# Kernel tuning notes

Measured on AMD Instinct MI355X. Metric: run time of the kernel, lower is better.

## Reference

```python
import jax, jax.numpy as jnp
import numpy as np

D_MODEL = 1024
N_HEADS = 16
HEAD_DIM = D_MODEL // N_HEADS
LN_EPS = 1e-6


def setup_inputs() -> dict:
    key = jax.random.key(0)
    ks = jax.random.split(key, 10)
    B, L, D = 4, 1024, D_MODEL
    s = 1.0 / np.sqrt(D)
    return {
        "q": jax.random.normal(ks[0], (B, L, D), jnp.float32),
        "k": jax.random.normal(ks[1], (B, L, D), jnp.float32),
        "v": jax.random.normal(ks[2], (B, L, D), jnp.float32),
        "masks": jnp.zeros((B, L, L), jnp.bool_),
        "Wq": jax.random.normal(ks[3], (D, D), jnp.float32) * s,
        "bq": jnp.zeros((D,), jnp.float32),
        "Wk": jax.random.normal(ks[4], (D, D), jnp.float32) * s,
        "bk": jnp.zeros((D,), jnp.float32),
        "Wv": jax.random.normal(ks[5], (D, D), jnp.float32) * s,
        "bv": jnp.zeros((D,), jnp.float32),
        "ln_g": jnp.ones((D,), jnp.float32),
        "ln_b": jnp.zeros((D,), jnp.float32),
    }


def _layer_norm(x, g, b):
    mu = jnp.mean(x, axis=-1, keepdims=True)
    var = jnp.var(x, axis=-1, keepdims=True)
    return (x - mu) * jax.lax.rsqrt(var + LN_EPS) * g + b


def reference(q, k, v, masks, Wq, bq, Wk, bk, Wv, bv, ln_g, ln_b):
    B, Lq, D = q.shape
    Lk = k.shape[1]
    H, Dh = N_HEADS, HEAD_DIM
    # linear projections (nn.Linear: x @ W.T + b)
    qp = q @ Wq.T + bq  # [B, Lq, D]
    kp = k @ Wk.T + bk
    vp = v @ Wv.T + bv
    # split heads: [B, L, D] -> [B, H, L, Dh]
    qh = qp.reshape(B, Lq, H, Dh).transpose(0, 2, 1, 3)
    kh = kp.reshape(B, Lk, H, Dh).transpose(0, 2, 1, 3)
    vh = vp.reshape(B, Lk, H, Dh).transpose(0, 2, 1, 3)
    scores = jnp.einsum("bhqd,bhkd->bhqk", qh, kh) / jnp.sqrt(jnp.float32(Dh))
    scores = jnp.where(masks[:, None, :, :], -jnp.inf, scores)
    attention = jax.nn.softmax(scores, axis=-1)  # [B, H, Lq, Lk]
    ctx = jnp.einsum("bhqk,bhkd->bhqd", attention, vh)  # [B, H, Lq, Dh]
    ctx = ctx.transpose(0, 2, 1, 3).reshape(B, Lq, D)  # unmulti_head
    output = _layer_norm(qp + ctx, ln_g, ln_b)  # residual is projected q
    return output, attention.reshape(B * H, Lq, Lk)
```

## Files before the change

### kernel.cpp

```cpp
#include <hip/hip_runtime.h>
#include <hip/hip_bf16.h>

typedef short bf16x8 __attribute__((ext_vector_type(8)));
typedef short bf16x4 __attribute__((ext_vector_type(4)));
typedef float f32x4 __attribute__((ext_vector_type(4)));
typedef unsigned short u16x8 __attribute__((ext_vector_type(8)));
typedef unsigned short u16x4 __attribute__((ext_vector_type(4)));

#define DEV static __device__ __forceinline__

DEV unsigned short f2bf(float f) {
  unsigned int u = __builtin_bit_cast(unsigned int, f);
  u += 0x7FFFu + ((u >> 16) & 1u);
  return (unsigned short)(u >> 16);
}
DEV float bf2f(unsigned short u) {
  return __builtin_bit_cast(float, (unsigned int)u << 16);
}

DEV void gload_lds16(const unsigned short* g, unsigned short* l) {
  __builtin_amdgcn_global_load_lds(
      (const __attribute__((address_space(1))) unsigned int*)g,
      (__attribute__((address_space(3))) unsigned int*)l, 16, 0, 0);
}

DEV void waitv(int n) {
  switch (n) {
    case 0: asm volatile("s_waitcnt vmcnt(0)" ::: "memory"); break;
    case 1: asm volatile("s_waitcnt vmcnt(1)" ::: "memory"); break;
    case 2: asm volatile("s_waitcnt vmcnt(2)" ::: "memory"); break;
    case 3: asm volatile("s_waitcnt vmcnt(3)" ::: "memory"); break;
    case 4: asm volatile("s_waitcnt vmcnt(4)" ::: "memory"); break;
    case 5: asm volatile("s_waitcnt vmcnt(5)" ::: "memory"); break;
    case 6: asm volatile("s_waitcnt vmcnt(6)" ::: "memory"); break;
    default: asm volatile("s_waitcnt vmcnt(0)" ::: "memory"); break;
  }
}

#define SB() __builtin_amdgcn_sched_barrier(0)
#define BAR() do { __builtin_amdgcn_s_barrier(); SB(); } while (0)
#define LBAR() do { asm volatile("s_waitcnt lgkmcnt(0)" ::: "memory"); \
                    SB(); \
                    __builtin_amdgcn_s_barrier(); \
                    SB(); } while (0)
#define WAITL() do { asm volatile("s_waitcnt lgkmcnt(0)" ::: "memory"); SB(); } while (0)
#define PRIO1() __builtin_amdgcn_s_setprio(1)
#define PRIO0() __builtin_amdgcn_s_setprio(0)

DEV void amask(unsigned mwv, f32x4& s) {
  if (mwv) {
#pragma unroll
    for (int r = 0; r < 4; ++r)
      if ((mwv >> (8 * r)) & 0xffu) s[r] = -1.0e30f;
  }
}

__global__ __launch_bounds__(256) void cvt_kernel(
    const float* __restrict__ q, const float* __restrict__ k,
    const float* __restrict__ v, const float* __restrict__ wq,
    const float* __restrict__ wk, const float* __restrict__ wv,
    unsigned short* __restrict__ xq, unsigned short* __restrict__ xk,
    unsigned short* __restrict__ xv, unsigned short* __restrict__ wqb,
    unsigned short* __restrict__ wkb, unsigned short* __restrict__ wvb)
{
  int tid = blockIdx.x * 256 + threadIdx.x;
  const float* src; unsigned short* dst; int off;
  if      (tid <  524288) { src = q;  dst = xq;  off = tid; }
  else if (tid < 1048576) { src = k;  dst = xk;  off = tid -  524288; }
  else if (tid < 1572864) { src = v;  dst = xv;  off = tid - 1048576; }
  else if (tid < 1703936) { src = wq; dst = wqb; off = tid - 1572864; }
  else if (tid < 1835008) { src = wk; dst = wkb; off = tid - 1703936; }
  else                    { src = wv; dst = wvb; off = tid - 1835008; }
  size_t e = (size_t)off * 8;
  float4 a = *(const float4*)(src + e);
  float4 b = *(const float4*)(src + e + 4);
  u16x8 p = { f2bf(a.x), f2bf(a.y), f2bf(a.z), f2bf(a.w),
              f2bf(b.x), f2bf(b.y), f2bf(b.z), f2bf(b.w) };
  *(u16x8*)(dst + e) = p;
}

__global__ __launch_bounds__(512, 2) void gemm_kernel(
    const unsigned short* __restrict__ xq, const unsigned short* __restrict__ xk,
    const unsigned short* __restrict__ xv, const unsigned short* __restrict__ wqb,
    const unsigned short* __restrict__ wkb, const unsigned short* __restrict__ wvb,
    const float* __restrict__ bq, const float* __restrict__ bk,
    const float* __restrict__ bv, unsigned short* __restrict__ qp,
    unsigned short* __restrict__ kp, unsigned short* __restrict__ vt)
{
  __shared__ union {
    unsigned short ab[2][2][128][64];
    unsigned short T[128][132];
  } smu;
  const int t = threadIdx.x, lane = t & 63, wv8 = t >> 6;
  const int ln = lane & 15, g = lane >> 4;
  const int wm2 = wv8 >> 2, wn4 = wv8 & 3;
  const int seg = blockIdx.x >> 8, lb = blockIdx.x & 255;
  const int x8 = lb & 7, s32 = lb >> 3;
  const int m0 = (x8 * 4 + (s32 >> 3)) * 128;
  const int n0 = (s32 & 7) * 128;

  const unsigned short* X; const unsigned short* W; const float* bias;
  unsigned short* outR; int mode;
  if (seg == 0)      { X = xq; W = wqb; bias = bq; outR = qp; mode = 0; }
  else if (seg == 1) { X = xk; W = wkb; bias = bk; outR = kp; mode = 0; }
  else               { X = xv; W = wvb; bias = bv; outR = vt; mode = 2; }

  f32x4 acc[4][2];
#pragma unroll
  for (int i = 0; i < 4; ++i)
#pragma unroll
    for (int j = 0; j < 2; ++j) acc[i][j] = {0.f, 0.f, 0.f, 0.f};

  const int lrow = lane >> 3;
  const int lcol = ((lane & 7) ^ lrow) * 8;

#define STAGE_G(kt) do { \
    const int _k0 = (kt) * 64; \
    _Pragma("unroll") \
    for (int i = 0; i < 2; ++i) { \
      const int r = wv8 * 16 + i * 8; \
      gload_lds16(X + (size_t)(m0 + r + lrow) * 1024 + _k0 + lcol, \
                  &smu.ab[(kt) & 1][0][r][0]); \
      gload_lds16(W + (size_t)(n0 + r + lrow) * 1024 + _k0 + lcol, \
                  &smu.ab[(kt) & 1][1][r][0]); \
    } } while (0)

  STAGE_G(0);
  waitv(0);
  BAR();
#pragma unroll 2
  for (int kt = 0; kt < 16; ++kt) {
    if (kt < 15) STAGE_G(kt + 1);
    SB();
#pragma unroll
    for (int ks = 0; ks < 2; ++ks) {
      bf16x8 af[4], bfr[2];
      const int ru = ((ks * 4 + g) ^ (ln & 7)) * 8;
#pragma unroll
      for (int i = 0; i < 4; ++i)
        af[i] = *(const bf16x8*)&smu.ab[kt & 1][0][wm2 * 64 + i * 16 + ln][ru];
#pragma unroll
      for (int j = 0; j < 2; ++j)
        bfr[j] = *(const bf16x8*)&smu.ab[kt & 1][1][wn4 * 32 + j * 16 + ln][ru];
      PRIO1();
#pragma unroll
      for (int i = 0; i < 4; ++i)
#pragma unroll
        for (int j = 0; j < 2; ++j)
          acc[i][j] = __builtin_amdgcn_mfma_f32_16x16x32_bf16(
              af[i], bfr[j], acc[i][j], 0, 0, 0);
      PRIO0();
    }
    SB();
    waitv(0);
    BAR();
  }

  float bvv[2];
#pragma unroll
  for (int j = 0; j < 2; ++j) bvv[j] = bias[n0 + wn4 * 32 + j * 16 + ln];

  if (mode == 0) {
#pragma unroll
    for (int i = 0; i < 4; ++i)
#pragma unroll
      for (int j = 0; j < 2; ++j)
#pragma unroll
        for (int r = 0; r < 4; ++r) {
          int row = m0 + wm2 * 64 + i * 16 + g * 4 + r;
          int col = n0 + wn4 * 32 + j * 16 + ln;
          outR[(size_t)row * 1024 + col] = f2bf(acc[i][j][r] + bvv[j]);
        }
  } else {
    __syncthreads();
#pragma unroll
    for (int i = 0; i < 4; ++i)
#pragma unroll
      for (int j = 0; j < 2; ++j)
#pragma unroll
        for (int r = 0; r < 4; ++r)
          smu.T[wn4 * 32 + j * 16 + ln][wm2 * 64 + i * 16 + g * 4 + r] =
              f2bf(acc[i][j][r] + bvv[j]);
    __syncthreads();
    const int bb = m0 >> 10, l0 = m0 & 1023;
#pragma unroll
    for (int it = 0; it < 4; ++it) {
      const int col = it * 32 + (t >> 4);
      const int r8 = (t & 15) * 8;
      *(u16x8*)&outR[((size_t)(bb * 16 + (n0 >> 6) + (col >> 6)) * 64 + (col & 63)) * 1024 + l0 + r8] =
          *(const u16x8*)&smu.T[col][r8];
    }
  }
#undef STAGE_G
}

__global__ __launch_bounds__(512, 2) void attn_kernel(
    const unsigned short* __restrict__ qp, const unsigned short* __restrict__ kp,
    const unsigned short* __restrict__ vt, const unsigned char* __restrict__ masks,
    float* __restrict__ attn_out, float* __restrict__ res_out)
{
  __shared__ union {
    unsigned short Kw[8][3][1024];
    unsigned short Vb[3][64][128];
    float ctxp[4][32][68];
  } sm;
  __shared__ float red[2][2][16][4];

  const int t = threadIdx.x;
  const int wv = t >> 6, lane = t & 63;
  const int ln = lane & 15, g = lane >> 4;
  const int wq = wv & 3, wm = wv >> 2;
  const int hw = blockIdx.x;
  const int lid = (hw & 7) * 256 + (hw >> 3);
  const int b = lid >> 9, h = (lid >> 5) & 15, m0 = (lid & 31) * 32;
  const size_t rowbase = (size_t)(b * 1024 + m0);

  bf16x8 qf[2];
  {
    const unsigned short* qb =
        qp + (rowbase + wm * 16 + ln) * 1024 + h * 64 + g * 8;
    qf[0] = *(const bf16x8*)qb;
    qf[1] = *(const bf16x8*)(qb + 32);
  }
  SB();

  const int slr8 = lane >> 3;
  const int suK = (lane & 7) ^ slr8;
  const int vlr = lane >> 4;
  const int vu1 = (lane & 15) ^ vlr;
  const int vu2 = (lane & 15) ^ (4 + vlr);
  const unsigned short* kbase = kp + (size_t)b * 1048576 + h * 64;
  const unsigned short* vtb = vt + ((size_t)(b * 16 + h) * 64) * 1024;
  unsigned short* kwv = &sm.Kw[wv][0][0];

#define STAGE_K(tt) do { \
    gload_lds16(kbase + (size_t)((tt) * 64 + wq * 16 + slr8) * 1024 + suK * 8, \
                kwv + ((tt) % 3) * 1024); \
    gload_lds16(kbase + (size_t)((tt) * 64 + wq * 16 + 8 + slr8) * 1024 + suK * 8, \
                kwv + ((tt) % 3) * 1024 + 512); } while (0)
#define STAGE_V(c) do { \
    gload_lds16(vtb + (size_t)(wv * 8 + vlr) * 1024 + (c) * 128 + vu1 * 8, \
                &sm.Vb[(c) % 3][wv * 8][0]); \
    gload_lds16(vtb + (size_t)(wv * 8 + 4 + vlr) * 1024 + (c) * 128 + vu2 * 8, \
                &sm.Vb[(c) % 3][wv * 8 + 4][0]); } while (0)

  f32x4 sc[16];
#pragma unroll
  for (int i = 0; i < 16; ++i) sc[i] = {0.f, 0.f, 0.f, 0.f};

  STAGE_K(0); STAGE_K(1); STAGE_K(2);
  SB();
#pragma unroll
  for (int tt = 0; tt < 16; ++tt) {
    waitv(tt <= 13 ? 4 : (tt == 14 ? 2 : 0));
    SB();
    const unsigned short* ksl = kwv + (tt % 3) * 1024 + ln * 64;
    bf16x8 kf0 = *(const bf16x8*)(ksl + (g ^ (ln & 7)) * 8);
    bf16x8 kf1 = *(const bf16x8*)(ksl + ((4 + g) ^ (ln & 7)) * 8);
    WAITL();
    if (tt + 3 < 16) STAGE_K(tt + 3);
    SB();
    PRIO1();
    sc[tt] = __builtin_amdgcn_mfma_f32_16x16x32_bf16(kf0, qf[0], sc[tt], 0, 0, 0);
    sc[tt] = __builtin_amdgcn_mfma_f32_16x16x32_bf16(kf1, qf[1], sc[tt], 0, 0, 0);
    PRIO0();
  }

  unsigned mw[16];
  {
    const unsigned char* mrow =
        masks + ((size_t)b * 1024 + m0 + wm * 16 + ln) * 1024 + wq * 16 + g * 4;
#pragma unroll
    for (int tt = 0; tt < 16; ++tt) mw[tt] = *(const unsigned*)(mrow + tt * 64);
  }
  SB();

  LBAR();
  STAGE_V(0); STAGE_V(1);
  SB();

  const float C = 0.18033688011112042f;
  float mx = -3.0e30f;
#pragma unroll
  for (int tt = 0; tt < 16; ++tt) {
    amask(mw[tt], sc[tt]);
#pragma unroll
    for (int r = 0; r < 4; ++r) mx = fmaxf(mx, sc[tt][r]);
  }
  mx = fmaxf(mx, __shfl_xor(mx, 16));
  mx = fmaxf(mx, __shfl_xor(mx, 32));
  const float mtl = mx * C;
  float sum = 0.f;
#pragma unroll
  for (int tt = 0; tt < 16; ++tt)
#pragma unroll
    for (int r = 0; r < 4; ++r)
      sum += exp2f(__builtin_fmaf(sc[tt][r], C, -mtl));
  sum += __shfl_xor(sum, 16);
  sum += __shfl_xor(sum, 32);
  if (g == 0) { red[0][wm][ln][wq] = mx; red[1][wm][ln][wq] = sum; }
  LBAR();
  float m4 = fmaxf(fmaxf(red[0][wm][ln][0], red[0][wm][ln][1]),
                   fmaxf(red[0][wm][ln][2], red[0][wm][ln][3]));
  float l4 = 0.f;
#pragma unroll
  for (int i = 0; i < 4; ++i)
    l4 += red[1][wm][ln][i] * exp2f((red[0][wm][ln][i] - m4) * C);
  const float beta = __builtin_fmaf(-m4, C, -__builtin_log2f(l4));

  bf16x8 af8[8];
#pragma unroll
  for (int c = 0; c < 8; ++c) {
    bf16x8 a;
#pragma unroll
    for (int r = 0; r < 4; ++r)
      a[r] = (short)f2bf(exp2f(__builtin_fmaf(sc[2 * c][r], C, beta)));
#pragma unroll
    for (int r = 0; r < 4; ++r)
      a[4 + r] = (short)f2bf(exp2f(__builtin_fmaf(sc[2 * c + 1][r], C, beta)));
    af8[c] = a;
  }

  f32x4 cacc[4];
#pragma unroll
  for (int i = 0; i < 4; ++i) cacc[i] = {0.f, 0.f, 0.f, 0.f};
#pragma unroll
  for (int c = 0; c < 8; ++c) {
    waitv(c <= 6 ? 2 : 0);
    BAR();
    if (c + 2 < 8) STAGE_V(c + 2);
    SB();
#pragma unroll
    for (int ni = 0; ni < 4; ++ni) {
      const int d = ni * 16 + ln;
      const int u0 = (2 * wq + (g >> 1)) ^ (ln & 7);
      const int u1 = (8 + 2 * wq + (g >> 1)) ^ (ln & 7);
      bf16x4 b0 = *(const bf16x4*)&sm.Vb[c % 3][d][u0 * 8 + (g & 1) * 4];
      bf16x4 b1 = *(const bf16x4*)&sm.Vb[c % 3][d][u1 * 8 + (g & 1) * 4];
      bf16x8 bfr = { b0[0], b0[1], b0[2], b0[3], b1[0], b1[1], b1[2], b1[3] };
      PRIO1();
      cacc[ni] = __builtin_amdgcn_mfma_f32_16x16x32_bf16(af8[c], bfr, cacc[ni], 0, 0, 0);
      PRIO0();
    }
    SB();
  }

  LBAR();
#pragma unroll
  for (int ni = 0; ni < 4; ++ni)
#pragma unroll
    for (int r = 0; r < 4; ++r)
      sm.ctxp[wq][wm * 16 + g * 4 + r][ni * 16 + ln] = cacc[ni][r];
  LBAR();
  {
    const int m = t >> 4, d4 = (t & 15) * 4;
    f32x4 s0 = *(const f32x4*)&sm.ctxp[0][m][d4];
    f32x4 s1 = *(const f32x4*)&sm.ctxp[1][m][d4];
    f32x4 s2 = *(const f32x4*)&sm.ctxp[2][m][d4];
    f32x4 s3 = *(const f32x4*)&sm.ctxp[3][m][d4];
    f32x4 s = s0 + s1 + s2 + s3;
    const unsigned short* qrow = qp + (rowbase + m) * 1024 + h * 64 + d4;
    u16x4 qv = *(const u16x4*)qrow;
    f32x4 qf32 = { bf2f(qv[0]), bf2f(qv[1]), bf2f(qv[2]), bf2f(qv[3]) };
    s = s + qf32;
    *(f32x4*)(res_out + (rowbase + m) * 1024 + h * 64 + d4) = s;
  }
  SB();

  {
    const size_t abase =
        ((size_t)(b * 16 + h) * 1024 + (m0 + wm * 16 + ln)) * 1024 + wq * 16 + g * 4;
#pragma unroll
    for (int c = 0; c < 8; ++c)
#pragma unroll
      for (int hf = 0; hf < 2; ++hf) {
        f32x4 v = { bf2f((unsigned short)af8[c][hf * 4 + 0]),
                    bf2f((unsigned short)af8[c][hf * 4 + 1]),
                    bf2f((unsigned short)af8[c][hf * 4 + 2]),
                    bf2f((unsigned short)af8[c][hf * 4 + 3]) };
        *(f32x4*)(attn_out + abase + (2 * c + hf) * 64) = v;
      }
  }
#undef STAGE_K
#undef STAGE_V
}

__global__ __launch_bounds__(256) void ln_kernel(
    float* __restrict__ io,
    const float* __restrict__ gma, const float* __restrict__ bta)
{
  __shared__ float rbuf[2][4];
  const int r = blockIdx.x, t = threadIdx.x;
  const int i4 = t * 4;
  const size_t base = (size_t)r * 1024 + i4;
  f32x4 x = *(const f32x4*)(io + base);
  float s = x[0] + x[1] + x[2] + x[3];
  float q = x[0]*x[0] + x[1]*x[1] + x[2]*x[2] + x[3]*x[3];
#pragma unroll
  for (int off = 1; off < 64; off <<= 1) {
    s += __shfl_xor(s, off);
    q += __shfl_xor(q, off);
  }
  const int wv = t >> 6;
  if ((t & 63) == 0) { rbuf[0][wv] = s; rbuf[1][wv] = q; }
  __syncthreads();
  s = rbuf[0][0] + rbuf[0][1] + rbuf[0][2] + rbuf[0][3];
  q = rbuf[1][0] + rbuf[1][1] + rbuf[1][2] + rbuf[1][3];
  float mu = s * (1.0f / 1024.0f);
  float var = q * (1.0f / 1024.0f) - mu * mu;
  float is = rsqrtf(var + 1e-6f);
  f32x4 gv = *(const f32x4*)(gma + i4);
  f32x4 bv = *(const f32x4*)(bta + i4);
  f32x4 o;
#pragma unroll
  for (int k = 0; k < 4; ++k) o[k] = (x[k] - mu) * is * gv[k] + bv[k];
  *(f32x4*)(io + base) = o;
}

extern "C" void kernel_launch(void* const* d_in, const int* in_sizes, int n_in,
                              void* d_out, int out_size, void* d_ws, size_t ws_size,
                              hipStream_t stream) {
  const float* q  = (const float*)d_in[0];
  const float* k  = (const float*)d_in[1];
  const float* v  = (const float*)d_in[2];
  const unsigned char* masks = (const unsigned char*)d_in[3];
  const float* Wq = (const float*)d_in[4];
  const float* bq = (const float*)d_in[5];
  const float* Wk = (const float*)d_in[6];
  const float* bk = (const float*)d_in[7];
  const float* Wv = (const float*)d_in[8];
  const float* bv = (const float*)d_in[9];
  const float* lg = (const float*)d_in[10];
  const float* lb = (const float*)d_in[11];

  float* out = (float*)d_out;
  float* attn_out = out + (size_t)4 * 1024 * 1024;

  unsigned short* xq  = (unsigned short*)attn_out;
  unsigned short* xk  = xq + 4194304;
  unsigned short* xv  = xk + 4194304;
  unsigned short* wqb = xv + 4194304;
  unsigned short* wkb = wqb + 1048576;
  unsigned short* wvb = wkb + 1048576;

  unsigned short* qp = (unsigned short*)d_ws;
  unsigned short* kp = qp + 4194304;
  unsigned short* vt = kp + 4194304;

  hipLaunchKernelGGL(cvt_kernel, dim3(7680), dim3(256), 0, stream,
                     q, k, v, Wq, Wk, Wv, xq, xk, xv, wqb, wkb, wvb);
  hipLaunchKernelGGL(gemm_kernel, dim3(768), dim3(512), 0, stream,
                     xq, xk, xv, wqb, wkb, wvb, bq, bk, bv, qp, kp, vt);
  hipLaunchKernelGGL(attn_kernel, dim3(2048), dim3(512), 0, stream,
                     qp, kp, vt, masks, attn_out, out);
  hipLaunchKernelGGL(ln_kernel, dim3(4096), dim3(256), 0, stream,
                     out, lg, lb);
}
```

Measured before the change: 184.4 us.

## Fuse activation bf16 conversion into GEMM loads and interleave attention-prob stores

```diff
diff --git a/kernel.cpp b/kernel.cpp
--- a/kernel.cpp
+++ b/kernel.cpp
@@ -55,22 +55,16 @@
   }
 }
 
-__global__ __launch_bounds__(256) void cvt_kernel(
-    const float* __restrict__ q, const float* __restrict__ k,
-    const float* __restrict__ v, const float* __restrict__ wq,
-    const float* __restrict__ wk, const float* __restrict__ wv,
-    unsigned short* __restrict__ xq, unsigned short* __restrict__ xk,
-    unsigned short* __restrict__ xv, unsigned short* __restrict__ wqb,
+__global__ __launch_bounds__(256) void cvtw_kernel(
+    const float* __restrict__ wq, const float* __restrict__ wk,
+    const float* __restrict__ wv, unsigned short* __restrict__ wqb,
     unsigned short* __restrict__ wkb, unsigned short* __restrict__ wvb)
 {
   int tid = blockIdx.x * 256 + threadIdx.x;
   const float* src; unsigned short* dst; int off;
-  if      (tid <  524288) { src = q;  dst = xq;  off = tid; }
-  else if (tid < 1048576) { src = k;  dst = xk;  off = tid -  524288; }
-  else if (tid < 1572864) { src = v;  dst = xv;  off = tid - 1048576; }
-  else if (tid < 1703936) { src = wq; dst = wqb; off = tid - 1572864; }
-  else if (tid < 1835008) { src = wk; dst = wkb; off = tid - 1703936; }
-  else                    { src = wv; dst = wvb; off = tid - 1835008; }
+  if      (tid < 131072) { src = wq; dst = wqb; off = tid; }
+  else if (tid < 262144) { src = wk; dst = wkb; off = tid - 131072; }
+  else                   { src = wv; dst = wvb; off = tid - 262144; }
   size_t e = (size_t)off * 8;
   float4 a = *(const float4*)(src + e);
   float4 b = *(const float4*)(src + e + 4);
@@ -80,8 +74,8 @@
 }
 
 __global__ __launch_bounds__(512, 2) void gemm_kernel(
-    const unsigned short* __restrict__ xq, const unsigned short* __restrict__ xk,
-    const unsigned short* __restrict__ xv, const unsigned short* __restrict__ wqb,
+    const float* __restrict__ xq, const float* __restrict__ xk,
+    const float* __restrict__ xv, const unsigned short* __restrict__ wqb,
     const unsigned short* __restrict__ wkb, const unsigned short* __restrict__ wvb,
     const float* __restrict__ bq, const float* __restrict__ bk,
     const float* __restrict__ bv, unsigned short* __restrict__ qp,
@@ -99,7 +93,7 @@
   const int m0 = (x8 * 4 + (s32 >> 3)) * 128;
   const int n0 = (s32 & 7) * 128;
 
-  const unsigned short* X; const unsigned short* W; const float* bias;
+  const float* X; const unsigned short* W; const float* bias;
   unsigned short* outR; int mode;
   if (seg == 0)      { X = xq; W = wqb; bias = bq; outR = qp; mode = 0; }
   else if (seg == 1) { X = xk; W = wkb; bias = bk; outR = kp; mode = 0; }
@@ -112,25 +106,41 @@
     for (int j = 0; j < 2; ++j) acc[i][j] = {0.f, 0.f, 0.f, 0.f};
 
   const int lrow = lane >> 3;
-  const int lcol = ((lane & 7) ^ lrow) * 8;
-
-#define STAGE_G(kt) do { \
-    const int _k0 = (kt) * 64; \
+  const int lu = lane & 7;
+  const int lcol = (lu ^ lrow) * 8;
+  const float* arow0 = X + (size_t)(m0 + wv8 * 16 + lrow) * 1024 + lcol;
+
+  float4 a0, a1, a2, a3;
+
+#define LOAD_A(kt) do { \
+    const float* _ga = arow0 + (kt) * 64; \
+    a0 = *(const float4*)_ga;  a1 = *(const float4*)(_ga + 4); \
+    a2 = *(const float4*)(_ga + 8192); a3 = *(const float4*)(_ga + 8196); \
+  } while (0)
+#define WRITE_A(kt) do { \
+    u16x8 _p0 = { f2bf(a0.x), f2bf(a0.y), f2bf(a0.z), f2bf(a0.w), \
+                  f2bf(a1.x), f2bf(a1.y), f2bf(a1.z), f2bf(a1.w) }; \
+    u16x8 _p1 = { f2bf(a2.x), f2bf(a2.y), f2bf(a2.z), f2bf(a2.w), \
+                  f2bf(a3.x), f2bf(a3.y), f2bf(a3.z), f2bf(a3.w) }; \
+    *(u16x8*)&smu.ab[(kt) & 1][0][wv8 * 16 + lrow][lu * 8] = _p0; \
+    *(u16x8*)&smu.ab[(kt) & 1][0][wv8 * 16 + 8 + lrow][lu * 8] = _p1; \
+  } while (0)
+#define STAGE_W(kt) do { \
     _Pragma("unroll") \
     for (int i = 0; i < 2; ++i) { \
       const int r = wv8 * 16 + i * 8; \
-      gload_lds16(X + (size_t)(m0 + r + lrow) * 1024 + _k0 + lcol, \
-                  &smu.ab[(kt) & 1][0][r][0]); \
-      gload_lds16(W + (size_t)(n0 + r + lrow) * 1024 + _k0 + lcol, \
+      gload_lds16(W + (size_t)(n0 + r + lrow) * 1024 + (kt) * 64 + lcol, \
                   &smu.ab[(kt) & 1][1][r][0]); \
     } } while (0)
 
-  STAGE_G(0);
+  STAGE_W(0);
+  LOAD_A(0);
   waitv(0);
-  BAR();
+  WRITE_A(0);
+  LBAR();
 #pragma unroll 2
   for (int kt = 0; kt < 16; ++kt) {
-    if (kt < 15) STAGE_G(kt + 1);
+    if (kt < 15) { STAGE_W(kt + 1); LOAD_A(kt + 1); }
     SB();
 #pragma unroll
     for (int ks = 0; ks < 2; ++ks) {
@@ -152,8 +162,12 @@
       PRIO0();
     }
     SB();
-    waitv(0);
-    BAR();
+    if (kt < 15) {
+      waitv(0);
+      SB();
+      WRITE_A(kt + 1);
+    }
+    LBAR();
   }
 
   float bvv[2];
@@ -191,7 +205,9 @@
           *(const u16x8*)&smu.T[col][r8];
     }
   }
-#undef STAGE_G
+#undef LOAD_A
+#undef WRITE_A
+#undef STAGE_W
 }
 
 __global__ __launch_bounds__(512, 2) void attn_kernel(
@@ -324,9 +340,11 @@
   f32x4 cacc[4];
 #pragma unroll
   for (int i = 0; i < 4; ++i) cacc[i] = {0.f, 0.f, 0.f, 0.f};
+  const size_t abase =
+      ((size_t)(b * 16 + h) * 1024 + (m0 + wm * 16 + ln)) * 1024 + wq * 16 + g * 4;
 #pragma unroll
   for (int c = 0; c < 8; ++c) {
-    waitv(c <= 6 ? 2 : 0);
+    waitv(c == 0 ? 2 : (c == 1 ? 4 : (c <= 6 ? 6 : 4)));
     BAR();
     if (c + 2 < 8) STAGE_V(c + 2);
     SB();
@@ -341,6 +359,15 @@
       PRIO1();
       cacc[ni] = __builtin_amdgcn_mfma_f32_16x16x32_bf16(af8[c], bfr, cacc[ni], 0, 0, 0);
       PRIO0();
+    }
+    SB();
+#pragma unroll
+    for (int hf = 0; hf < 2; ++hf) {
+      f32x4 v = { bf2f((unsigned short)af8[c][hf * 4 + 0]),
+                  bf2f((unsigned short)af8[c][hf * 4 + 1]),
+                  bf2f((unsigned short)af8[c][hf * 4 + 2]),
+                  bf2f((unsigned short)af8[c][hf * 4 + 3]) };
+      *(f32x4*)(attn_out + abase + (2 * c + hf) * 64) = v;
     }
     SB();
   }
@@ -365,22 +392,6 @@
     s = s + qf32;
     *(f32x4*)(res_out + (rowbase + m) * 1024 + h * 64 + d4) = s;
   }
-  SB();
-
-  {
-    const size_t abase =
-        ((size_t)(b * 16 + h) * 1024 + (m0 + wm * 16 + ln)) * 1024 + wq * 16 + g * 4;
-#pragma unroll
-    for (int c = 0; c < 8; ++c)
-#pragma unroll
-      for (int hf = 0; hf < 2; ++hf) {
-        f32x4 v = { bf2f((unsigned short)af8[c][hf * 4 + 0]),
-                    bf2f((unsigned short)af8[c][hf * 4 + 1]),
-                    bf2f((unsigned short)af8[c][hf * 4 + 2]),
-                    bf2f((unsigned short)af8[c][hf * 4 + 3]) };
-        *(f32x4*)(attn_out + abase + (2 * c + hf) * 64) = v;
-      }
-  }
 #undef STAGE_K
 #undef STAGE_V
 }
@@ -436,10 +447,7 @@
   float* out = (float*)d_out;
   float* attn_out = out + (size_t)4 * 1024 * 1024;
 
-  unsigned short* xq  = (unsigned short*)attn_out;
-  unsigned short* xk  = xq + 4194304;
-  unsigned short* xv  = xk + 4194304;
-  unsigned short* wqb = xv + 4194304;
+  unsigned short* wqb = (unsigned short*)attn_out;
   unsigned short* wkb = wqb + 1048576;
   unsigned short* wvb = wkb + 1048576;
 
@@ -447,10 +455,10 @@
   unsigned short* kp = qp + 4194304;
   unsigned short* vt = kp + 4194304;
 
-  hipLaunchKernelGGL(cvt_kernel, dim3(7680), dim3(256), 0, stream,
-                     q, k, v, Wq, Wk, Wv, xq, xk, xv, wqb, wkb, wvb);
+  hipLaunchKernelGGL(cvtw_kernel, dim3(1536), dim3(256), 0, stream,
+                     Wq, Wk, Wv, wqb, wkb, wvb);
   hipLaunchKernelGGL(gemm_kernel, dim3(768), dim3(512), 0, stream,
-                     xq, xk, xv, wqb, wkb, wvb, bq, bk, bv, qp, kp, vt);
+                     q, k, v, wqb, wkb, wvb, bq, bk, bv, qp, kp, vt);
   hipLaunchKernelGGL(attn_kernel, dim3(2048), dim3(512), 0, stream,
                      qp, kp, vt, masks, attn_out, out);
   hipLaunchKernelGGL(ln_kernel, dim3(4096), dim3(256), 0, stream,
```

Measured after the change: 189.7 us. 1.03x slower.
